# Kernel tuning notes

Measured on AMD Instinct MI355X. Metric: run time of the kernel, lower is better.

Reference implementation:

```python
import jax, jax.numpy as jnp
import numpy as np

D = 1024
H = 16
DH = D // H  # 64
SCALE = DH ** (-0.5)

def setup_inputs() -> dict:
    key = jax.random.key(0)
    k1, k2, k3, k4, k5 = jax.random.split(key, 5)
    x = jax.random.normal(k1, (4, 2048, D), dtype=jnp.float32)
    w_qkv = jax.random.normal(k2, (D, 3 * D), dtype=jnp.float32) * (D ** -0.5)
    b_qkv = jax.random.normal(k3, (3 * D,), dtype=jnp.float32) * 0.02
    w_out = jax.random.normal(k4, (D, D), dtype=jnp.float32) * (D ** -0.5)
    b_out = jax.random.normal(k5, (D,), dtype=jnp.float32) * 0.02
    return {"x": x, "w_qkv": w_qkv, "b_qkv": b_qkv, "w_out": w_out, "b_out": b_out}

def reference(x, w_qkv, b_qkv, w_out, b_out):
    B, S, C = x.shape
    qkv = x @ w_qkv + b_qkv                          # [B,S,3D]
    qkv = qkv.reshape(B, S, 3, H, DH)
    qkv = jnp.transpose(qkv, (0, 3, 2, 1, 4))        # [B,H,3,S,DH]
    q, k, v = qkv[:, :, 0], qkv[:, :, 1], qkv[:, :, 2]
    q = q * SCALE
    scores = jnp.einsum('bhqd,bhkd->bhqk', q, k)     # [B,H,S,S]
    attn = jax.nn.softmax(scores.astype(jnp.float32), axis=-1).astype(scores.dtype)
    out = jnp.einsum('bhqk,bhkd->bhqd', attn, v)     # [B,H,S,DH]
    out = jnp.transpose(out, (0, 2, 1, 3)).reshape(B, S, C)
    return out @ w_out + b_out
```

## Files before the change

### kernel.cpp

```cpp
#include <hip/hip_runtime.h>

#define D_ 1024
#define H_ 16
#define DH_ 64
#define S_ 2048
#define B_ 4
#define N_ (B_*S_)
#define M3_ 3072
#define QSC_ 0.18033688011112042f

typedef _Float16 f16;
typedef _Float16 f16x8 __attribute__((ext_vector_type(8)));
typedef _Float16 f16x4 __attribute__((ext_vector_type(4)));
typedef _Float16 f16x2 __attribute__((ext_vector_type(2)));
typedef __fp16   h16x2 __attribute__((ext_vector_type(2)));
typedef float    f32x4 __attribute__((ext_vector_type(4)));

typedef __attribute__((address_space(1))) void gvoid;
typedef __attribute__((address_space(3))) void lvoid;

__device__ __forceinline__ void gl16(const f16* g, f16* l) {
    __builtin_amdgcn_global_load_lds((gvoid*)g, (lvoid*)l, 16, 0, 0);
}

__device__ __forceinline__ f16x2 pk_cvt(float a, float b) {
#if __has_builtin(__builtin_amdgcn_cvt_pkrtz)
    h16x2 t = __builtin_amdgcn_cvt_pkrtz(a, b);
    return __builtin_bit_cast(f16x2, t);
#else
    f16x2 r; r[0] = (f16)a; r[1] = (f16)b; return r;
#endif
}

__global__ __launch_bounds__(256) void prep_kernel(
        const float* __restrict__ x,  f16* __restrict__ xb,
        const float* __restrict__ wq, f16* __restrict__ wqT,
        const float* __restrict__ wo, f16* __restrict__ woT) {
    __shared__ float tile[32][33];
    const int bid = blockIdx.x;
    if (bid < 8192) {
        size_t i = ((size_t)bid * 256 + threadIdx.x) * 4;
        float4 f = *reinterpret_cast<const float4*>(x + i);
        f16x4 o;
        o[0] = (f16)f.x; o[1] = (f16)f.y; o[2] = (f16)f.z; o[3] = (f16)f.w;
        *reinterpret_cast<f16x4*>(xb + i) = o;
        return;
    }
    const float* in; f16* out; int Nc, bx, by;
    if (bid < 11264) {
        int t = bid - 8192;  in = wq; out = wqT; Nc = M3_;
        bx = t % 96; by = t / 96;
    } else {
        int t = bid - 11264; in = wo; out = woT; Nc = D_;
        bx = t & 31; by = t >> 5;
    }
    int tx = threadIdx.x & 31, ty = threadIdx.x >> 5;
    int c = bx * 32 + tx;
    #pragma unroll
    for (int i = 0; i < 4; i++) {
        int r = by * 32 + ty + i * 8;
        tile[ty + i * 8][tx] = in[(size_t)r * Nc + c];
    }
    __syncthreads();
    #pragma unroll
    for (int i = 0; i < 4; i++) {
        int r2 = bx * 32 + ty + i * 8;
        int c2 = by * 32 + tx;
        out[(size_t)r2 * D_ + c2] = (f16)tile[tx][ty + i * 8];
    }
}

__global__ __launch_bounds__(256, 3) void gemm_qkv_kernel(
        const f16* __restrict__ A, const f16* __restrict__ Bt,
        const float* __restrict__ bias,
        f16* __restrict__ qo, f16* __restrict__ ko, f16* __restrict__ vTo) {
    __shared__ __align__(16) f16 As[2][128 * 32];
    __shared__ __align__(16) f16 Bs[2][128 * 32];
    const int tid  = threadIdx.x;
    const int lane = tid & 63, w = tid >> 6;
    const int quad = lane >> 4, lrow = lane & 15;
    const int wm = (w & 1) * 64, wn = (w >> 1) * 64;
    const int id  = blockIdx.x;
    const int xcd = id & 7, idx = id >> 3;
    const int n0 = (xcd * 8 + (idx & 7)) * 128;
    const int m0 = (idx >> 3) * 128;

    f32x4 acc[4][4];
    #pragma unroll
    for (int i = 0; i < 4; i++)
        #pragma unroll
        for (int j = 0; j < 4; j++) acc[i][j] = {0.f, 0.f, 0.f, 0.f};

    const int ar0 = tid >> 2, ap0 = tid & 3;
    const f16* Ag0 = A  + (size_t)(n0 + ar0) * D_ + ap0 * 8;
    const f16* Ag1 = Ag0 + (size_t)64 * D_;
    const f16* Bg0 = Bt + (size_t)(m0 + ar0) * D_ + ap0 * 8;
    const f16* Bg1 = Bg0 + (size_t)64 * D_;

    gl16(Ag0, &As[0][tid * 8]);
    gl16(Ag1, &As[0][tid * 8 + 64 * 32]);
    gl16(Bg0, &Bs[0][tid * 8]);
    gl16(Bg1, &Bs[0][tid * 8 + 64 * 32]);
    __syncthreads();

    for (int kt = 0; kt < 32; kt++) {
        const int cur = kt & 1;
        if (kt + 1 < 32) {
            const int ko = (kt + 1) * 32;
            gl16(Ag0 + ko, &As[cur ^ 1][tid * 8]);
            gl16(Ag1 + ko, &As[cur ^ 1][tid * 8 + 64 * 32]);
            gl16(Bg0 + ko, &Bs[cur ^ 1][tid * 8]);
            gl16(Bg1 + ko, &Bs[cur ^ 1][tid * 8 + 64 * 32]);
        }
        f16x8 af[4], bf[4];
        #pragma unroll
        for (int i = 0; i < 4; i++)
            af[i] = *reinterpret_cast<const f16x8*>(&As[cur][(wm + i * 16 + lrow) * 32 + quad * 8]);
        #pragma unroll
        for (int j = 0; j < 4; j++)
            bf[j] = *reinterpret_cast<const f16x8*>(&Bs[cur][(wn + j * 16 + lrow) * 32 + quad * 8]);
        __builtin_amdgcn_s_setprio(1);
        #pragma unroll
        for (int i = 0; i < 4; i++)
            #pragma unroll
            for (int j = 0; j < 4; j++)
                acc[i][j] = __builtin_amdgcn_mfma_f32_16x16x32_f16(af[i], bf[j], acc[i][j], 0, 0, 0);
        __builtin_amdgcn_s_setprio(0);
        __syncthreads();
    }

    #pragma unroll
    for (int j = 0; j < 4; j++) {
        int m   = m0 + wn + j * 16 + lrow;
        int sec = m >> 10;
        int hd  = m & 1023;
        int hh  = hd >> 6, d = hd & 63;
        float bb = bias[m];
        if (sec == 2) {
            #pragma unroll
            for (int i = 0; i < 4; i++) {
                int n = n0 + wm + i * 16 + quad * 4;
                int bidx = n >> 11, s = n & 2047;
                f16x4 o;
                #pragma unroll
                for (int r = 0; r < 4; r++) o[r] = (f16)(acc[i][j][r] + bb);
                *reinterpret_cast<f16x4*>(
                    &vTo[(((size_t)(bidx * H_ + hh)) * DH_ + d) * S_ + s]) = o;
            }
        } else {
            f16* dst = (sec == 0) ? qo : ko;
            float sc = (sec == 0) ? QSC_ : 1.0f;
            #pragma unroll
            for (int i = 0; i < 4; i++) {
                #pragma unroll
                for (int r = 0; r < 4; r++) {
                    int n = n0 + wm + i * 16 + quad * 4 + r;
                    int bidx = n >> 11, s = n & 2047;
                    dst[(((size_t)(bidx * H_ + hh)) * S_ + s) * DH_ + d] =
                        (f16)((acc[i][j][r] + bb) * sc);
                }
            }
        }
    }
}

__global__ __launch_bounds__(256, 4) void attn_kernel(
        const f16* __restrict__ q, const f16* __restrict__ k,
        const f16* __restrict__ vT, f16* __restrict__ ctx) {
    __shared__ __align__(16) f16 Ks[2][64 * 64];
    __shared__ __align__(16) f16 Vs[2][64 * 64];
    const int tid  = threadIdx.x;
    const int lane = tid & 63, w = tid >> 6;
    const int quad = lane >> 4, lrow = lane & 15;
    const int id = blockIdx.x;
    const int bh = id & 63;
    const int q0 = (id >> 6) * 128;
    const int b  = bh >> 4, h = bh & 15;
    const f16* qb = q  + (size_t)bh * S_ * DH_;
    const f16* kb = k  + (size_t)bh * S_ * DH_;
    const f16* vb = vT + (size_t)bh * DH_ * S_;

    f16x8 qf[2][2];
    #pragma unroll
    for (int f = 0; f < 2; f++)
        #pragma unroll
        for (int hf = 0; hf < 2; hf++)
            qf[f][hf] = *reinterpret_cast<const f16x8*>(
                qb + (size_t)(q0 + w * 32 + f * 16 + lrow) * DH_ + hf * 32 + quad * 8);

    f16x8 ones8;
    #pragma unroll
    for (int i = 0; i < 8; i++) ones8[i] = (f16)1.f;

    f32x4 lacc[2];
    f32x4 ot[2][4];
    #pragma unroll
    for (int f = 0; f < 2; f++) {
        lacc[f] = {0.f, 0.f, 0.f, 0.f};
        #pragma unroll
        for (int dj = 0; dj < 4; dj++) ot[f][dj] = {0.f, 0.f, 0.f, 0.f};
    }

    int koff[2], voff[2];
    #pragma unroll
    for (int i = 0; i < 2; i++) {
        int c = i * 256 + tid;
        int s = c >> 3, p = c & 7;
        int g = (s & ~31) | (((s >> 2) & 3) << 3) | (((s >> 4) & 1) << 2) | (s & 3);
        koff[i] = g * DH_ + ((p ^ (s & 7)) * 8);
        voff[i] = s * S_ + ((p ^ (s & 7)) * 8);
    }

    #pragma unroll
    for (int i = 0; i < 2; i++) {
        gl16(kb + koff[i], &Ks[0][(i * 256 + tid) * 8]);
        gl16(vb + voff[i], &Vs[0][(i * 256 + tid) * 8]);
    }
    __syncthreads();

    const int xr0 = (quad ^ (lrow & 7)) * 8;
    const int xr1 = ((quad + 4) ^ (lrow & 7)) * 8;

    union PU { f16x8 v; f16x2 w[4]; };

    const int NT = S_ / 64;
    for (int kt = 0; kt < NT; kt++) {
        const int cur = kt & 1;
        const f16* Kc = Ks[cur];
        const f16* Vc = Vs[cur];

        f32x4 st0[2][2];
        __builtin_amdgcn_s_setprio(1);
        #pragma unroll
        for (int half = 0; half < 2; half++) {
            const int rb = (half * 16 + lrow) * 64;
            const f16x8 k0 = *reinterpret_cast<const f16x8*>(&Kc[rb + xr0]);
            const f16x8 k1 = *reinterpret_cast<const f16x8*>(&Kc[rb + xr1]);
            #pragma unroll
            for (int f = 0; f < 2; f++) {
                f32x4 s = {0.f, 0.f, 0.f, 0.f};
                s = __builtin_amdgcn_mfma_f32_16x16x32_f16(k0, qf[f][0], s, 0, 0, 0);
                s = __builtin_amdgcn_mfma_f32_16x16x32_f16(k1, qf[f][1], s, 0, 0, 0);
                st0[half][f] = s;
            }
        }
        __builtin_amdgcn_s_setprio(0);

        if (kt + 1 < NT) {
            const size_t kv1 = (size_t)(kt + 1) * 64;
            #pragma unroll
            for (int i = 0; i < 2; i++) {
                gl16(kb + kv1 * DH_ + koff[i], &Ks[cur ^ 1][(i * 256 + tid) * 8]);
                gl16(vb + kv1 + voff[i],       &Vs[cur ^ 1][(i * 256 + tid) * 8]);
            }
        }

        PU p0[2];
        #pragma unroll
        for (int half = 0; half < 2; half++)
            #pragma unroll
            for (int f = 0; f < 2; f++) {
                f16x2 lo = pk_cvt(__builtin_amdgcn_exp2f(st0[half][f][0]),
                                  __builtin_amdgcn_exp2f(st0[half][f][1]));
                f16x2 hi = pk_cvt(__builtin_amdgcn_exp2f(st0[half][f][2]),
                                  __builtin_amdgcn_exp2f(st0[half][f][3]));
                p0[f].w[half * 2 + 0] = lo;
                p0[f].w[half * 2 + 1] = hi;
            }

        f32x4 st1[2][2];
        __builtin_amdgcn_s_setprio(1);
        #pragma unroll
        for (int half = 0; half < 2; half++) {
            const int rb = ((2 + half) * 16 + lrow) * 64;
            const f16x8 k0 = *reinterpret_cast<const f16x8*>(&Kc[rb + xr0]);
            const f16x8 k1 = *reinterpret_cast<const f16x8*>(&Kc[rb + xr1]);
            #pragma unroll
            for (int f = 0; f < 2; f++) {
                f32x4 s = {0.f, 0.f, 0.f, 0.f};
                s = __builtin_amdgcn_mfma_f32_16x16x32_f16(k0, qf[f][0], s, 0, 0, 0);
                s = __builtin_amdgcn_mfma_f32_16x16x32_f16(k1, qf[f][1], s, 0, 0, 0);
                st1[half][f] = s;
            }
        }
        __builtin_amdgcn_s_setprio(0);

        f16x8 vf0[4];
        #pragma unroll
        for (int dj = 0; dj < 4; dj++)
            vf0[dj] = *reinterpret_cast<const f16x8*>(
                &Vc[(dj * 16 + lrow) * 64 + ((quad ^ (lrow & 7)) * 8)]);

        __builtin_amdgcn_s_setprio(1);
        #pragma unroll
        for (int dj = 0; dj < 4; dj++)
            #pragma unroll
            for (int f = 0; f < 2; f++)
                ot[f][dj] = __builtin_amdgcn_mfma_f32_16x16x32_f16(vf0[dj], p0[f].v, ot[f][dj], 0, 0, 0);
        #pragma unroll
        for (int f = 0; f < 2; f++)
            lacc[f] = __builtin_amdgcn_mfma_f32_16x16x32_f16(ones8, p0[f].v, lacc[f], 0, 0, 0);
        __builtin_amdgcn_s_setprio(0);

        PU p1[2];
        #pragma unroll
        for (int half = 0; half < 2; half++)
            #pragma unroll
            for (int f = 0; f < 2; f++) {
                f16x2 lo = pk_cvt(__builtin_amdgcn_exp2f(st1[half][f][0]),
                                  __builtin_amdgcn_exp2f(st1[half][f][1]));
                f16x2 hi = pk_cvt(__builtin_amdgcn_exp2f(st1[half][f][2]),
                                  __builtin_amdgcn_exp2f(st1[half][f][3]));
                p1[f].w[half * 2 + 0] = lo;
                p1[f].w[half * 2 + 1] = hi;
            }

        f16x8 vf1[4];
        #pragma unroll
        for (int dj = 0; dj < 4; dj++)
            vf1[dj] = *reinterpret_cast<const f16x8*>(
                &Vc[(dj * 16 + lrow) * 64 + (((4 + quad) ^ (lrow & 7)) * 8)]);

        __builtin_amdgcn_s_setprio(1);
        #pragma unroll
        for (int dj = 0; dj < 4; dj++)
            #pragma unroll
            for (int f = 0; f < 2; f++)
                ot[f][dj] = __builtin_amdgcn_mfma_f32_16x16x32_f16(vf1[dj], p1[f].v, ot[f][dj], 0, 0, 0);
        #pragma unroll
        for (int f = 0; f < 2; f++)
            lacc[f] = __builtin_amdgcn_mfma_f32_16x16x32_f16(ones8, p1[f].v, lacc[f], 0, 0, 0);
        __builtin_amdgcn_s_setprio(0);

        __syncthreads();
    }

    #pragma unroll
    for (int f = 0; f < 2; f++) {
        float inv = 1.0f / lacc[f][0];
        int qrow = q0 + w * 32 + f * 16 + lrow;
        #pragma unroll
        for (int dj = 0; dj < 4; dj++) {
            f16x4 o;
            #pragma unroll
            for (int r = 0; r < 4; r++) o[r] = (f16)(ot[f][dj][r] * inv);
            *reinterpret_cast<f16x4*>(
                &ctx[((size_t)(b * S_ + qrow)) * D_ + h * DH_ + dj * 16 + quad * 4]) = o;
        }
    }
}

__global__ __launch_bounds__(256, 3) void gemm_out_kernel(
        const f16* __restrict__ A, const f16* __restrict__ Bt,
        const float* __restrict__ bias, float* __restrict__ out) {
    __shared__ __align__(16) f16 As[2][128 * 32];
    __shared__ __align__(16) f16 Bs[2][128 * 32];
    const int tid  = threadIdx.x;
    const int lane = tid & 63, w = tid >> 6;
    const int quad = lane >> 4, lrow = lane & 15;
    const int wm = (w & 1) * 64, wn = (w >> 1) * 64;
    const int id  = blockIdx.x;
    const int xcd = id & 7, idx = id >> 3;
    const int n0 = (xcd * 8 + (idx & 7)) * 128;
    const int m0 = (idx >> 3) * 128;

    f32x4 acc[4][4];
    #pragma unroll
    for (int i = 0; i < 4; i++)
        #pragma unroll
        for (int j = 0; j < 4; j++) acc[i][j] = {0.f, 0.f, 0.f, 0.f};

    const int ar0 = tid >> 2, ap0 = tid & 3;
    const f16* Ag0 = A  + (size_t)(n0 + ar0) * D_ + ap0 * 8;
    const f16* Ag1 = Ag0 + (size_t)64 * D_;
    const f16* Bg0 = Bt + (size_t)(m0 + ar0) * D_ + ap0 * 8;
    const f16* Bg1 = Bg0 + (size_t)64 * D_;

    gl16(Ag0, &As[0][tid * 8]);
    gl16(Ag1, &As[0][tid * 8 + 64 * 32]);
    gl16(Bg0, &Bs[0][tid * 8]);
    gl16(Bg1, &Bs[0][tid * 8 + 64 * 32]);
    __syncthreads();

    for (int kt = 0; kt < 32; kt++) {
        const int cur = kt & 1;
        if (kt + 1 < 32) {
            const int ko = (kt + 1) * 32;
            gl16(Ag0 + ko, &As[cur ^ 1][tid * 8]);
            gl16(Ag1 + ko, &As[cur ^ 1][tid * 8 + 64 * 32]);
            gl16(Bg0 + ko, &Bs[cur ^ 1][tid * 8]);
            gl16(Bg1 + ko, &Bs[cur ^ 1][tid * 8 + 64 * 32]);
        }
        f16x8 af[4], bf[4];
        #pragma unroll
        for (int i = 0; i < 4; i++)
            af[i] = *reinterpret_cast<const f16x8*>(&As[cur][(wm + i * 16 + lrow) * 32 + quad * 8]);
        #pragma unroll
        for (int j = 0; j < 4; j++)
            bf[j] = *reinterpret_cast<const f16x8*>(&Bs[cur][(wn + j * 16 + lrow) * 32 + quad * 8]);
        __builtin_amdgcn_s_setprio(1);
        #pragma unroll
        for (int i = 0; i < 4; i++)
            #pragma unroll
            for (int j = 0; j < 4; j++)
                acc[i][j] = __builtin_amdgcn_mfma_f32_16x16x32_f16(af[i], bf[j], acc[i][j], 0, 0, 0);
        __builtin_amdgcn_s_setprio(0);
        __syncthreads();
    }

    #pragma unroll
    for (int j = 0; j < 4; j++) {
        int m = m0 + wn + j * 16 + lrow;
        float bb = bias[m];
        #pragma unroll
        for (int i = 0; i < 4; i++)
            #pragma unroll
            for (int r = 0; r < 4; r++) {
                int n = n0 + wm + i * 16 + quad * 4 + r;
                out[(size_t)n * D_ + m] = acc[i][j][r] + bb;
            }
    }
}

extern "C" void kernel_launch(void* const* d_in, const int* in_sizes, int n_in,
                              void* d_out, int out_size, void* d_ws, size_t ws_size,
                              hipStream_t stream) {
    (void)in_sizes; (void)n_in; (void)out_size; (void)ws_size;
    const float* x     = (const float*)d_in[0];
    const float* w_qkv = (const float*)d_in[1];
    const float* b_qkv = (const float*)d_in[2];
    const float* w_out = (const float*)d_in[3];
    const float* b_out = (const float*)d_in[4];
    float* out = (float*)d_out;

    char* ws = (char*)d_ws;
    const size_t MB = 1024 * 1024;
    f16* xb    = (f16*)(ws);
    f16* wqkvT = (f16*)(ws + 16 * MB);
    f16* woutT = (f16*)(ws + 22 * MB);
    f16* qs    = (f16*)(ws + 24 * MB);
    f16* kk    = (f16*)(ws + 40 * MB);
    f16* vTb   = (f16*)(ws + 72 * MB);
    f16* ctx   = xb;

    prep_kernel<<<12288, 256, 0, stream>>>(x, xb, w_qkv, wqkvT, w_out, woutT);
    gemm_qkv_kernel<<<1536, 256, 0, stream>>>(xb, wqkvT, b_qkv, qs, kk, vTb);
    attn_kernel<<<(B_ * H_) * (S_ / 128), 256, 0, stream>>>(qs, kk, vTb, ctx);
    gemm_out_kernel<<<512, 256, 0, stream>>>(ctx, woutT, b_out, out);
}
```

Before: 268.8 us.

## Fuse x fp32-to-fp16 conversion into QKV GEMM load and move attention barrier

Removes the separate x conversion pass from prep_kernel; the QKV GEMM now loads fp32 x tiles into registers, packs them to fp16 and stores into LDS after the MFMAs, avoiding a full write and re-read of the fp16 copy. The attention loop replaces its trailing __syncthreads with an explicit waitcnt plus barrier placed before the PV MFMAs. The trade-off is doubled A-operand traffic in the GEMM (fp32 reads repeated across column blocks) and register-staged loads instead of direct-to-LDS loads.

After: 273.1 us. No clear change (+1.6%).

```diff
diff --git a/kernel.cpp b/kernel.cpp
--- a/kernel.cpp
+++ b/kernel.cpp
@@ -32,26 +32,27 @@
 #endif
 }
 
+union PK8 { f16x8 v; f16x2 h[4]; };
+__device__ __forceinline__ f16x8 pack8(float4 lo, float4 hi) {
+    PK8 u;
+    u.h[0] = pk_cvt(lo.x, lo.y);
+    u.h[1] = pk_cvt(lo.z, lo.w);
+    u.h[2] = pk_cvt(hi.x, hi.y);
+    u.h[3] = pk_cvt(hi.z, hi.w);
+    return u.v;
+}
+
 __global__ __launch_bounds__(256) void prep_kernel(
-        const float* __restrict__ x,  f16* __restrict__ xb,
         const float* __restrict__ wq, f16* __restrict__ wqT,
         const float* __restrict__ wo, f16* __restrict__ woT) {
     __shared__ float tile[32][33];
     const int bid = blockIdx.x;
-    if (bid < 8192) {
-        size_t i = ((size_t)bid * 256 + threadIdx.x) * 4;
-        float4 f = *reinterpret_cast<const float4*>(x + i);
-        f16x4 o;
-        o[0] = (f16)f.x; o[1] = (f16)f.y; o[2] = (f16)f.z; o[3] = (f16)f.w;
-        *reinterpret_cast<f16x4*>(xb + i) = o;
-        return;
-    }
     const float* in; f16* out; int Nc, bx, by;
-    if (bid < 11264) {
-        int t = bid - 8192;  in = wq; out = wqT; Nc = M3_;
-        bx = t % 96; by = t / 96;
+    if (bid < 3072) {
+        in = wq; out = wqT; Nc = M3_;
+        bx = bid % 96; by = bid / 96;
     } else {
-        int t = bid - 11264; in = wo; out = woT; Nc = D_;
+        int t = bid - 3072; in = wo; out = woT; Nc = D_;
         bx = t & 31; by = t >> 5;
     }
     int tx = threadIdx.x & 31, ty = threadIdx.x >> 5;
@@ -71,7 +72,7 @@
 }
 
 __global__ __launch_bounds__(256, 3) void gemm_qkv_kernel(
-        const f16* __restrict__ A, const f16* __restrict__ Bt,
+        const float* __restrict__ X, const f16* __restrict__ Bt,
         const float* __restrict__ bias,
         f16* __restrict__ qo, f16* __restrict__ ko, f16* __restrict__ vTo) {
     __shared__ __align__(16) f16 As[2][128 * 32];
@@ -92,23 +93,32 @@
         for (int j = 0; j < 4; j++) acc[i][j] = {0.f, 0.f, 0.f, 0.f};
 
     const int ar0 = tid >> 2, ap0 = tid & 3;
-    const f16* Ag0 = A  + (size_t)(n0 + ar0) * D_ + ap0 * 8;
-    const f16* Ag1 = Ag0 + (size_t)64 * D_;
-    const f16* Bg0 = Bt + (size_t)(m0 + ar0) * D_ + ap0 * 8;
-    const f16* Bg1 = Bg0 + (size_t)64 * D_;
-
-    gl16(Ag0, &As[0][tid * 8]);
-    gl16(Ag1, &As[0][tid * 8 + 64 * 32]);
-    gl16(Bg0, &Bs[0][tid * 8]);
-    gl16(Bg1, &Bs[0][tid * 8 + 64 * 32]);
+    const float* Ag0 = X  + (size_t)(n0 + ar0) * D_ + ap0 * 8;
+    const float* Ag1 = Ag0 + (size_t)64 * D_;
+    const f16*   Bg0 = Bt + (size_t)(m0 + ar0) * D_ + ap0 * 8;
+    const f16*   Bg1 = Bg0 + (size_t)64 * D_;
+
+    {
+        float4 a00 = *reinterpret_cast<const float4*>(Ag0);
+        float4 a01 = *reinterpret_cast<const float4*>(Ag0 + 4);
+        float4 a10 = *reinterpret_cast<const float4*>(Ag1);
+        float4 a11 = *reinterpret_cast<const float4*>(Ag1 + 4);
+        gl16(Bg0, &Bs[0][tid * 8]);
+        gl16(Bg1, &Bs[0][tid * 8 + 64 * 32]);
+        *reinterpret_cast<f16x8*>(&As[0][tid * 8])           = pack8(a00, a01);
+        *reinterpret_cast<f16x8*>(&As[0][tid * 8 + 64 * 32]) = pack8(a10, a11);
+    }
     __syncthreads();
 
     for (int kt = 0; kt < 32; kt++) {
         const int cur = kt & 1;
+        float4 a00, a01, a10, a11;
         if (kt + 1 < 32) {
             const int ko = (kt + 1) * 32;
-            gl16(Ag0 + ko, &As[cur ^ 1][tid * 8]);
-            gl16(Ag1 + ko, &As[cur ^ 1][tid * 8 + 64 * 32]);
+            a00 = *reinterpret_cast<const float4*>(Ag0 + ko);
+            a01 = *reinterpret_cast<const float4*>(Ag0 + ko + 4);
+            a10 = *reinterpret_cast<const float4*>(Ag1 + ko);
+            a11 = *reinterpret_cast<const float4*>(Ag1 + ko + 4);
             gl16(Bg0 + ko, &Bs[cur ^ 1][tid * 8]);
             gl16(Bg1 + ko, &Bs[cur ^ 1][tid * 8 + 64 * 32]);
         }
@@ -126,6 +136,10 @@
             for (int j = 0; j < 4; j++)
                 acc[i][j] = __builtin_amdgcn_mfma_f32_16x16x32_f16(af[i], bf[j], acc[i][j], 0, 0, 0);
         __builtin_amdgcn_s_setprio(0);
+        if (kt + 1 < 32) {
+            *reinterpret_cast<f16x8*>(&As[cur ^ 1][tid * 8])           = pack8(a00, a01);
+            *reinterpret_cast<f16x8*>(&As[cur ^ 1][tid * 8 + 64 * 32]) = pack8(a10, a11);
+        }
         __syncthreads();
     }
 
@@ -321,6 +335,10 @@
             vf1[dj] = *reinterpret_cast<const f16x8*>(
                 &Vc[(dj * 16 + lrow) * 64 + (((4 + quad) ^ (lrow & 7)) * 8)]);
 
+        asm volatile("s_waitcnt vmcnt(0) lgkmcnt(0)" ::: "memory");
+        __builtin_amdgcn_s_barrier();
+        __builtin_amdgcn_sched_barrier(0);
+
         __builtin_amdgcn_s_setprio(1);
         #pragma unroll
         for (int dj = 0; dj < 4; dj++)
@@ -331,8 +349,6 @@
         for (int f = 0; f < 2; f++)
             lacc[f] = __builtin_amdgcn_mfma_f32_16x16x32_f16(ones8, p1[f].v, lacc[f], 0, 0, 0);
         __builtin_amdgcn_s_setprio(0);
-
-        __syncthreads();
     }
 
     #pragma unroll
@@ -435,16 +451,15 @@
 
     char* ws = (char*)d_ws;
     const size_t MB = 1024 * 1024;
-    f16* xb    = (f16*)(ws);
+    f16* ctx   = (f16*)(ws);
     f16* wqkvT = (f16*)(ws + 16 * MB);
     f16* woutT = (f16*)(ws + 22 * MB);
     f16* qs    = (f16*)(ws + 24 * MB);
     f16* kk    = (f16*)(ws + 40 * MB);
     f16* vTb   = (f16*)(ws + 72 * MB);
-    f16* ctx   = xb;
-
-    prep_kernel<<<12288, 256, 0, stream>>>(x, xb, w_qkv, wqkvT, w_out, woutT);
-    gemm_qkv_kernel<<<1536, 256, 0, stream>>>(xb, wqkvT, b_qkv, qs, kk, vTb);
+
+    prep_kernel<<<4096, 256, 0, stream>>>(w_qkv, wqkvT, w_out, woutT);
+    gemm_qkv_kernel<<<1536, 256, 0, stream>>>(x, wqkvT, b_qkv, qs, kk, vTb);
     attn_kernel<<<(B_ * H_) * (S_ / 128), 256, 0, stream>>>(qs, kk, vTb, ctx);
     gemm_out_kernel<<<512, 256, 0, stream>>>(ctx, woutT, b_out, out);
 }
```
